# Optimization experiments

Hardware: AMD Instinct MI355X
Metric: run time of the kernel (lower is better)

Reference implementation:

```python
import jax, jax.numpy as jnp
import numpy as np

N, NS, C_IN, C_OUT = 20000, 32, 64, 128
V = (0.1, 0.1, 0.2)
BN_EPS = 1e-5


def setup_inputs() -> dict:
    key = jax.random.key(0)
    ks = jax.random.split(key, 5)
    features = jax.random.normal(ks[0], (N, NS, C_IN), jnp.float32)
    coords = jax.random.normal(ks[1], (N, NS, 3), jnp.float32)
    centers = jax.random.normal(ks[2], (N, 4), jnp.float32)
    mask = jax.random.randint(ks[3], (N, NS), 0, 2, jnp.int32)
    # Linear(C_IN, C_OUT, bias=False) weight, torch layout [out, in]
    W = jax.random.normal(ks[4], (C_OUT, C_IN), jnp.float32) / np.sqrt(C_IN)
    gamma = jnp.ones((C_OUT,), jnp.float32)   # BatchNorm1d weight
    beta = jnp.zeros((C_OUT,), jnp.float32)   # BatchNorm1d bias
    return dict(features=features, coords=coords, centers=centers, mask=mask,
                W=W, gamma=gamma, beta=beta)


def reference(features, coords, centers, mask, W, gamma, beta):
    # --- geometric features (no_grad in original) ---
    normalizer = jnp.array([V[0], V[1], V[2], V[0]**2 + V[1]**2 + V[2]**2],
                           dtype=jnp.float32)
    rel = coords - centers[:, 1:4][:, None, :]            # [N, NS, 3]
    dist = jnp.sum(rel * rel, axis=2, keepdims=True)       # [N, NS, 1]
    geo = jnp.concatenate([rel, dist], axis=2) / normalizer  # [N, NS, 4]

    # --- shared MLP: Linear -> BatchNorm1d (training stats) -> ReLU ---
    x = jnp.einsum('nsc,dc->nsd', features, W)             # [N, NS, C_OUT]
    xf = x.reshape(-1, C_OUT)
    mu = jnp.mean(xf, axis=0)
    var = jnp.mean((xf - mu) ** 2, axis=0)                 # biased var (torch BN)
    x = (x - mu) * jax.lax.rsqrt(var + BN_EPS) * gamma + beta
    x = jax.nn.relu(x)                                     # [N, NS, C_OUT]

    # --- weighted, masked mean pool over neighbors ---
    geo_rep = jnp.tile(geo, (1, 1, C_OUT // 4))            # [N, NS, C_OUT]
    m = mask.astype(jnp.float32)                           # [N, NS]
    num = jnp.sum(x * geo_rep * m[:, :, None], axis=1)     # [N, C_OUT]
    den = jnp.maximum(jnp.sum(m, axis=1, keepdims=True), 1.0)
    return num / den
```

## Files before the change

### kernel.cpp

```cpp
#include <hip/hip_runtime.h>
#include <hip/hip_bf16.h>

#define N_PTS 20000
#define NSAMP 32
#define CIN 64
#define COUT 128
#define M_ROWS (N_PTS * NSAMP)
#define TILES (M_ROWS / 64)
#define K1_BLOCKS 1250
#define K1_WAVES (K1_BLOCKS * 4)
#define SP_CHUNKS 25
#define SP_DEPTH 50
#define CP_CHUNKS 50
#define CP_DEPTH 100
#define BN_EPS 1e-5f

typedef __attribute__((ext_vector_type(8))) short short8v;
typedef __attribute__((ext_vector_type(4))) float f32x4;

__device__ inline short bf16_of(float f) {
    unsigned u = __float_as_uint(f);
    u = (u + 0x7FFFu + ((u >> 16) & 1u)) >> 16;
    return (short)u;
}

__global__ __launch_bounds__(256) void k1_stats(const float* __restrict__ F,
                                                float* __restrict__ Sp,
                                                float* __restrict__ Cp) {
    const int tid = threadIdx.x;
    const int wid = tid >> 6;
    const int lane = tid & 63;
    const int g = lane >> 4;
    const int i = lane & 15;
    const int gw = blockIdx.x * 4 + wid;

    f32x4 acc[4][4];
#pragma unroll
    for (int a = 0; a < 4; ++a)
#pragma unroll
        for (int b = 0; b < 4; ++b)
            acc[a][b] = (f32x4){0.f, 0.f, 0.f, 0.f};
    float colp[4] = {0.f, 0.f, 0.f, 0.f};

    for (int tile = gw; tile < TILES; tile += K1_WAVES) {
        const float* fb0 = F + (size_t)tile * 4096 + g * 512 + i;
        const float* fb1 = fb0 + 2048;
        short8v frag[4][2];
#pragma unroll
        for (int jt = 0; jt < 4; ++jt) {
            float cs = 0.f;
#pragma unroll
            for (int kk = 0; kk < 2; ++kk) {
                const float* p = kk ? fb1 : fb0;
                short8v fr;
#pragma unroll
                for (int r = 0; r < 8; ++r) {
                    float v = p[r * 64 + jt * 16];
                    cs += v;
                    fr[r] = bf16_of(v);
                }
                frag[jt][kk] = fr;
            }
            colp[jt] += cs;
        }
#pragma unroll
        for (int it = 0; it < 4; ++it)
#pragma unroll
            for (int jt = 0; jt < 4; ++jt) {
                acc[it][jt] = __builtin_amdgcn_mfma_f32_16x16x32_bf16(
                    frag[it][0], frag[jt][0], acc[it][jt], 0, 0, 0);
                acc[it][jt] = __builtin_amdgcn_mfma_f32_16x16x32_bf16(
                    frag[it][1], frag[jt][1], acc[it][jt], 0, 0, 0);
            }
    }

#pragma unroll
    for (int jt = 0; jt < 4; ++jt) {
        colp[jt] += __shfl_xor(colp[jt], 16);
        colp[jt] += __shfl_xor(colp[jt], 32);
    }
    if (lane < 16) {
#pragma unroll
        for (int jt = 0; jt < 4; ++jt)
            Cp[gw * 64 + jt * 16 + lane] = colp[jt];
    }

    __shared__ float sS[4096];
    for (int w = 0; w < 4; ++w) {
        if (wid == w) {
#pragma unroll
            for (int it = 0; it < 4; ++it)
#pragma unroll
                for (int jt = 0; jt < 4; ++jt)
#pragma unroll
                    for (int r = 0; r < 4; ++r) {
                        int idx = (it * 16 + g * 4 + r) * 64 + jt * 16 + i;
                        if (w == 0) sS[idx] = acc[it][jt][r];
                        else        sS[idx] += acc[it][jt][r];
                    }
        }
        __syncthreads();
    }
    float4* dst = (float4*)(Sp + (size_t)blockIdx.x * 4096);
    const float4* src = (const float4*)sS;
#pragma unroll
    for (int q = 0; q < 4; ++q)
        dst[q * 256 + tid] = src[q * 256 + tid];
}

__global__ __launch_bounds__(256) void kRedA(const float* __restrict__ Sp,
                                             const float* __restrict__ Cp,
                                             float* __restrict__ Tp,
                                             float* __restrict__ Tcp) {
    int t = blockIdx.x * 256 + threadIdx.x;
    if (t < SP_CHUNKS * 4096) {
        int o = t & 4095;
        int c = t >> 12;
        float s = 0.f;
#pragma unroll 10
        for (int b = 0; b < SP_DEPTH; ++b)
            s += Sp[(size_t)(c * SP_DEPTH + b) * 4096 + o];
        Tp[t] = s;
    } else if (t < SP_CHUNKS * 4096 + CP_CHUNKS * 64) {
        int u = t - SP_CHUNKS * 4096;
        int col = u & 63;
        int c = u >> 6;
        float s = 0.f;
#pragma unroll 10
        for (int w = 0; w < CP_DEPTH; ++w)
            s += Cp[(c * CP_DEPTH + w) * 64 + col];
        Tcp[u] = s;
    }
}

__global__ __launch_bounds__(256) void kRedB(const float* __restrict__ Tp,
                                             const float* __restrict__ Tcp,
                                             float* __restrict__ S,
                                             float* __restrict__ colsum) {
    int t = blockIdx.x * 256 + threadIdx.x;
    if (t < 4096) {
        float s = 0.f;
#pragma unroll
        for (int c = 0; c < SP_CHUNKS; ++c) s += Tp[c * 4096 + t];
        S[t] = s;
    } else if (t < 4160) {
        int col = t - 4096;
        float s = 0.f;
#pragma unroll
        for (int c = 0; c < CP_CHUNKS; ++c) s += Tcp[c * 64 + col];
        colsum[col] = s;
    }
}

__global__ __launch_bounds__(64) void k1_scales(const float* __restrict__ S,
                                                const float* __restrict__ colsum,
                                                const float* __restrict__ W,
                                                const float* __restrict__ gamma,
                                                const float* __restrict__ beta,
                                                float* __restrict__ scale,
                                                float* __restrict__ shift) {
    int d = blockIdx.x;
    int tid = threadIdx.x;
    __shared__ float w[64];
    w[tid] = W[d * 64 + tid];
    __syncthreads();
    float wi = w[tid];
    float rowdot = 0.f;
#pragma unroll
    for (int j = 0; j < 64; ++j) rowdot += S[tid * 64 + j] * w[j];
    float p = wi * rowdot;
    float mup = wi * colsum[tid];
    for (int k = 1; k <= 32; k <<= 1) {
        p += __shfl_xor(p, k);
        mup += __shfl_xor(mup, k);
    }
    if (tid == 0) {
        const float invM = 1.f / (float)M_ROWS;
        float mu = mup * invM;
        float ex2 = p * invM;
        float var = ex2 - mu * mu;
        float rs = rsqrtf(var + BN_EPS);
        float sc = gamma[d] * rs;
        scale[d] = sc;
        shift[d] = beta[d] - mu * sc;
    }
}

__global__ __launch_bounds__(256) void k2_main(const float* __restrict__ F,
                                               const float* __restrict__ coords,
                                               const float* __restrict__ centers,
                                               const int* __restrict__ mask,
                                               const float* __restrict__ W,
                                               const float* __restrict__ scale,
                                               const float* __restrict__ shift,
                                               float* __restrict__ out) {
    const int tid = threadIdx.x;
    const int wid = tid >> 6;
    const int lane = tid & 63;
    const int g = lane >> 4;
    const int i = lane & 15;
    const int n_base = (blockIdx.x * 4 + wid) * 4;

    short8v b[8][2];
#pragma unroll
    for (int t = 0; t < 8; ++t)
#pragma unroll
        for (int kk = 0; kk < 2; ++kk) {
            const float* wp = W + (t * 16 + i) * 64 + kk * 32 + g * 8;
            short8v fr;
#pragma unroll
            for (int r = 0; r < 8; ++r) fr[r] = bf16_of(wp[r]);
            b[t][kk] = fr;
        }
    float sc[8], sh[8];
#pragma unroll
    for (int t = 0; t < 8; ++t) {
        sc[t] = scale[t * 16 + i];
        sh[t] = shift[t * 16 + i];
    }

    __shared__ float geoM[4][32][4];
    const f32x4 Z = {0.f, 0.f, 0.f, 0.f};

    for (int it = 0; it < 4; ++it) {
        const int n = n_base + it;

        short8v a[2][2];
#pragma unroll
        for (int mt = 0; mt < 2; ++mt)
#pragma unroll
            for (int kk = 0; kk < 2; ++kk) {
                const float* fp =
                    F + ((size_t)n * NSAMP + mt * 16 + i) * 64 + kk * 32 + g * 8;
                short8v fr;
#pragma unroll
                for (int r = 0; r < 8; ++r) fr[r] = bf16_of(fp[r]);
                a[mt][kk] = fr;
            }

        float m = 0.f;
        if (lane < 32) {
            const int s = lane;
            const float* cp = coords + ((size_t)n * NSAMP + s) * 3;
            float r0 = cp[0] - centers[n * 4 + 1];
            float r1 = cp[1] - centers[n * 4 + 2];
            float r2 = cp[2] - centers[n * 4 + 3];
            float dist = r0 * r0 + r1 * r1 + r2 * r2;
            m = (float)mask[n * NSAMP + s];
            float4 gm = make_float4(r0 * 10.f * m, r1 * 10.f * m,
                                    r2 * 5.f * m, dist * (1.f / 0.06f) * m);
            *(float4*)&geoM[wid][s][0] = gm;
        }
        float den = m;
        for (int k = 1; k <= 32; k <<= 1) den += __shfl_xor(den, k);
        float inv_den = 1.f / fmaxf(den, 1.f);

        __builtin_amdgcn_sched_barrier(0x7F);

        float gv[2][4];
        const int j0 = i & 3;
#pragma unroll
        for (int mt = 0; mt < 2; ++mt)
#pragma unroll
            for (int r = 0; r < 4; ++r)
                gv[mt][r] = geoM[wid][mt * 16 + g * 4 + r][j0];

#pragma unroll
        for (int t = 0; t < 8; ++t) {
            float nump = 0.f;
#pragma unroll
            for (int mt = 0; mt < 2; ++mt) {
                f32x4 acc = __builtin_amdgcn_mfma_f32_16x16x32_bf16(
                    a[mt][0], b[t][0], Z, 0, 0, 0);
                acc = __builtin_amdgcn_mfma_f32_16x16x32_bf16(
                    a[mt][1], b[t][1], acc, 0, 0, 0);
#pragma unroll
                for (int r = 0; r < 4; ++r) {
                    float v = fmaf(acc[r], sc[t], sh[t]);
                    v = fmaxf(v, 0.f);
                    nump = fmaf(v, gv[mt][r], nump);
                }
            }
            nump += __shfl_xor(nump, 16);
            nump += __shfl_xor(nump, 32);
            if (lane < 16)
                out[(size_t)n * COUT + t * 16 + lane] = nump * inv_den;
        }
    }
}

extern "C" void kernel_launch(void* const* d_in, const int* in_sizes, int n_in,
                              void* d_out, int out_size, void* d_ws, size_t ws_size,
                              hipStream_t stream) {
    const float* F = (const float*)d_in[0];
    const float* coords = (const float*)d_in[1];
    const float* centers = (const float*)d_in[2];
    const int* mask = (const int*)d_in[3];
    const float* W = (const float*)d_in[4];
    const float* gamma = (const float*)d_in[5];
    const float* beta = (const float*)d_in[6];
    float* out = (float*)d_out;

    float* wsf = (float*)d_ws;
    float* scale = wsf;
    float* shift = wsf + 128;
    float* S = wsf + 256;
    float* colsum = wsf + 4352;
    float* Tp = wsf + 4416;
    float* Tcp = Tp + SP_CHUNKS * 4096;
    float* Sp = Tcp + CP_CHUNKS * 64;
    float* Cp = Sp + (size_t)K1_BLOCKS * 4096;

    k1_stats<<<K1_BLOCKS, 256, 0, stream>>>(F, Sp, Cp);
    kRedA<<<413, 256, 0, stream>>>(Sp, Cp, Tp, Tcp);
    kRedB<<<17, 256, 0, stream>>>(Tp, Tcp, S, colsum);
    k1_scales<<<COUT, 64, 0, stream>>>(S, colsum, W, gamma, beta, scale, shift);
    k2_main<<<1250, 256, 0, stream>>>(F, coords, centers, mask, W, scale, shift, out);
}
```

Before: 96.05 us.

## Fuse BN statistics stages into one cooperative kernel with grid syncs

Replaces the four-kernel statistics pipeline (Gram/colsum partials, two reduction passes, scale computation) with a single cooperative kernel of 500 blocks that uses grid.sync between phases. Fewer blocks each process more tiles, which shrinks the partial buffers, and the separate launches and their gaps go away. The cost is grid-wide barriers and less parallelism in the reduction phases, where only 64 or 128 blocks work while the rest wait. The old path is kept as a fallback if the cooperative launch fails.

```diff
diff --git a/kernel.cpp b/kernel.cpp
--- a/kernel.cpp
+++ b/kernel.cpp
@@ -1,5 +1,8 @@
 #include <hip/hip_runtime.h>
 #include <hip/hip_bf16.h>
+#include <hip/hip_cooperative_groups.h>
+
+namespace cg = cooperative_groups;
 
 #define N_PTS 20000
 #define NSAMP 32
@@ -7,13 +10,17 @@
 #define COUT 128
 #define M_ROWS (N_PTS * NSAMP)
 #define TILES (M_ROWS / 64)
+#define BN_EPS 1e-5f
+
+#define CBLOCKS 500
+#define CWAVES (CBLOCKS * 4)
+
 #define K1_BLOCKS 1250
 #define K1_WAVES (K1_BLOCKS * 4)
 #define SP_CHUNKS 25
 #define SP_DEPTH 50
 #define CP_CHUNKS 50
 #define CP_DEPTH 100
-#define BN_EPS 1e-5f
 
 typedef __attribute__((ext_vector_type(8))) short short8v;
 typedef __attribute__((ext_vector_type(4))) float f32x4;
@@ -22,6 +29,153 @@
     unsigned u = __float_as_uint(f);
     u = (u + 0x7FFFu + ((u >> 16) & 1u)) >> 16;
     return (short)u;
+}
+
+__global__ __launch_bounds__(256, 4) void coop_stats(
+    const float* __restrict__ F, const float* __restrict__ W,
+    const float* __restrict__ gamma, const float* __restrict__ beta,
+    float* __restrict__ scale, float* __restrict__ shift,
+    float* __restrict__ S, float* __restrict__ Sp, float* __restrict__ Cp) {
+    cg::grid_group grid = cg::this_grid();
+
+    const int tid = threadIdx.x;
+    const int wid = tid >> 6;
+    const int lane = tid & 63;
+    const int g = lane >> 4;
+    const int i = lane & 15;
+    const int bid = blockIdx.x;
+    const int gw = bid * 4 + wid;
+
+    __shared__ float sS[4096];
+    __shared__ float sC[4][64];
+    __shared__ float sw[64];
+
+    {
+        f32x4 acc[4][4];
+#pragma unroll
+        for (int a = 0; a < 4; ++a)
+#pragma unroll
+            for (int b = 0; b < 4; ++b)
+                acc[a][b] = (f32x4){0.f, 0.f, 0.f, 0.f};
+        float colp[4] = {0.f, 0.f, 0.f, 0.f};
+
+        for (int tile = gw; tile < TILES; tile += CWAVES) {
+            const float* fb0 = F + (size_t)tile * 4096 + g * 512 + i;
+            const float* fb1 = fb0 + 2048;
+            short8v frag[4][2];
+#pragma unroll
+            for (int jt = 0; jt < 4; ++jt) {
+                float cs = 0.f;
+#pragma unroll
+                for (int kk = 0; kk < 2; ++kk) {
+                    const float* p = kk ? fb1 : fb0;
+                    short8v fr;
+#pragma unroll
+                    for (int r = 0; r < 8; ++r) {
+                        float v = p[r * 64 + jt * 16];
+                        cs += v;
+                        fr[r] = bf16_of(v);
+                    }
+                    frag[jt][kk] = fr;
+                }
+                colp[jt] += cs;
+            }
+#pragma unroll
+            for (int it = 0; it < 4; ++it)
+#pragma unroll
+                for (int jt = 0; jt < 4; ++jt) {
+                    acc[it][jt] = __builtin_amdgcn_mfma_f32_16x16x32_bf16(
+                        frag[it][0], frag[jt][0], acc[it][jt], 0, 0, 0);
+                    acc[it][jt] = __builtin_amdgcn_mfma_f32_16x16x32_bf16(
+                        frag[it][1], frag[jt][1], acc[it][jt], 0, 0, 0);
+                }
+        }
+
+#pragma unroll
+        for (int jt = 0; jt < 4; ++jt) {
+            colp[jt] += __shfl_xor(colp[jt], 16);
+            colp[jt] += __shfl_xor(colp[jt], 32);
+        }
+        if (lane < 16) {
+#pragma unroll
+            for (int jt = 0; jt < 4; ++jt)
+                Cp[gw * 64 + jt * 16 + lane] = colp[jt];
+        }
+
+        for (int w = 0; w < 4; ++w) {
+            if (wid == w) {
+#pragma unroll
+                for (int it = 0; it < 4; ++it)
+#pragma unroll
+                    for (int jt = 0; jt < 4; ++jt)
+#pragma unroll
+                        for (int r = 0; r < 4; ++r) {
+                            int idx = (it * 16 + g * 4 + r) * 64 + jt * 16 + i;
+                            if (w == 0) sS[idx] = acc[it][jt][r];
+                            else        sS[idx] += acc[it][jt][r];
+                        }
+            }
+            __syncthreads();
+        }
+        float4* dst = (float4*)(Sp + (size_t)bid * 4096);
+        const float4* src = (const float4*)sS;
+#pragma unroll
+        for (int q = 0; q < 4; ++q)
+            dst[q * 256 + tid] = src[q * 256 + tid];
+    }
+    grid.sync();
+
+    {
+        float s1 = 0.f;
+        if (bid < 64) {
+            const size_t base = (size_t)(wid * 125) * 4096 + bid * 64 + lane;
+#pragma unroll 5
+            for (int p = 0; p < 125; ++p) s1 += Sp[base + (size_t)p * 4096];
+        }
+        __syncthreads();
+        sC[wid][lane] = s1;
+        __syncthreads();
+        if (bid < 64 && tid < 64)
+            S[bid * 64 + tid] =
+                sC[0][tid] + sC[1][tid] + sC[2][tid] + sC[3][tid];
+    }
+    grid.sync();
+
+    if (bid < COUT) {
+        float csp = 0.f;
+        {
+            const int base = wid * 500;
+#pragma unroll 5
+            for (int p = 0; p < 500; ++p) csp += Cp[(base + p) * 64 + lane];
+        }
+        __syncthreads();
+        sC[wid][lane] = csp;
+        if (tid < 64) sw[tid] = W[bid * 64 + tid];
+        __syncthreads();
+        if (tid < 64) {
+            float w_t = sw[tid];
+            float rowdot = 0.f;
+#pragma unroll
+            for (int j = 0; j < 64; ++j) rowdot += S[tid * 64 + j] * sw[j];
+            float cs = sC[0][tid] + sC[1][tid] + sC[2][tid] + sC[3][tid];
+            float pp = w_t * rowdot;
+            float mup = w_t * cs;
+            for (int k = 1; k <= 32; k <<= 1) {
+                pp += __shfl_xor(pp, k);
+                mup += __shfl_xor(mup, k);
+            }
+            if (tid == 0) {
+                const float invM = 1.f / (float)M_ROWS;
+                float mu = mup * invM;
+                float ex2 = pp * invM;
+                float var = ex2 - mu * mu;
+                float rs = rsqrtf(var + BN_EPS);
+                float sc = gamma[bid] * rs;
+                scale[bid] = sc;
+                shift[bid] = beta[bid] - mu * sc;
+            }
+        }
+    }
 }
 
 __global__ __launch_bounds__(256) void k1_stats(const float* __restrict__ F,
@@ -308,12 +462,28 @@
     float* colsum = wsf + 4352;
     float* Tp = wsf + 4416;
     float* Tcp = Tp + SP_CHUNKS * 4096;
-    float* Sp = Tcp + CP_CHUNKS * 64;
-    float* Cp = Sp + (size_t)K1_BLOCKS * 4096;
-
-    k1_stats<<<K1_BLOCKS, 256, 0, stream>>>(F, Sp, Cp);
-    kRedA<<<413, 256, 0, stream>>>(Sp, Cp, Tp, Tcp);
-    kRedB<<<17, 256, 0, stream>>>(Tp, Tcp, S, colsum);
-    k1_scales<<<COUT, 64, 0, stream>>>(S, colsum, W, gamma, beta, scale, shift);
-    k2_main<<<1250, 256, 0, stream>>>(F, coords, centers, mask, W, scale, shift, out);
-}
+    float* SpC = Tcp + CP_CHUNKS * 64;
+    float* CpC = SpC + (size_t)CBLOCKS * 4096;
+    float* SpF = CpC + (size_t)CWAVES * 64;
+    float* CpF = SpF + (size_t)K1_BLOCKS * 4096;
+
+    const float* Fc = F; const float* Wc = W;
+    const float* gc = gamma; const float* bc = beta;
+    float* scc = scale; float* shc = shift;
+    float* Sc = S; float* Spc = SpC; float* Cpc = CpC;
+    void* kargs[] = {(void*)&Fc,  (void*)&Wc,  (void*)&gc, (void*)&bc,
+                     (void*)&scc, (void*)&shc, (void*)&Sc, (void*)&Spc,
+                     (void*)&Cpc};
+    hipError_t err = hipLaunchCooperativeKernel(
+        (const void*)coop_stats, dim3(CBLOCKS), dim3(256), kargs, 0, stream);
+
+    if (err != hipSuccess) {
+        k1_stats<<<K1_BLOCKS, 256, 0, stream>>>(F, SpF, CpF);
+        kRedA<<<413, 256, 0, stream>>>(SpF, CpF, Tp, Tcp);
+        kRedB<<<17, 256, 0, stream>>>(Tp, Tcp, S, colsum);
+        k1_scales<<<COUT, 64, 0, stream>>>(S, colsum, W, gamma, beta, scale,
+                                           shift);
+    }
+    k2_main<<<1250, 256, 0, stream>>>(F, coords, centers, mask, W, scale,
+                                      shift, out);
+}
```

After: 272.5 us. +183.8%, slower.
